# Kernel optimization log

Measured on AMD Instinct MI355X. Metric: run time of the kernel, lower is better.

Reference implementation:

```python
import jax, jax.numpy as jnp
import numpy as np

B, T, IN, H, O = 128, 512, 512, 512, 128

def setup_inputs() -> dict:
    key = jax.random.key(0)
    ks = jax.random.split(key, 16)
    s = 1.0 / np.sqrt(H)
    u = lambda k, shape: jax.random.uniform(k, shape, jnp.float32, -s, s)
    return {
        "x": jax.random.normal(ks[0], (B, T, IN), jnp.float32),
        # PyTorch GRU layer 0: weight_ih_l0 [3H, IN] (gate order r,z,n)
        "W_ih0": u(ks[1], (3 * H, IN)), "W_hh0": u(ks[2], (3 * H, H)),
        "b_ih0": u(ks[3], (3 * H,)),   "b_hh0": u(ks[4], (3 * H,)),
        # layer 1
        "W_ih1": u(ks[5], (3 * H, H)), "W_hh1": u(ks[6], (3 * H, H)),
        "b_ih1": u(ks[7], (3 * H,)),   "b_hh1": u(ks[8], (3 * H,)),
        # fc: Linear(H, O); fc_cate: Linear(O, 3O)
        "W_fc": u(ks[9], (O, H)),      "b_fc": u(ks[10], (O,)),
        "W_fcc": jax.random.uniform(ks[11], (3 * O, O), jnp.float32, -1/np.sqrt(O), 1/np.sqrt(O)),
        "b_fcc": jax.random.uniform(ks[12], (3 * O,), jnp.float32, -1/np.sqrt(O), 1/np.sqrt(O)),
    }

def _gru_layer(x, W_ih, W_hh, b_ih, b_hh):
    # x: [B, T, D] -> hidden sequence [B, T, H]. PyTorch gate order: r, z, n.
    Bm, Tm, _ = x.shape
    Hm = W_hh.shape[1]
    # precompute input projections for all timesteps: [B, T, 3H]
    xg = jnp.einsum('btd,gd->btg', x, W_ih) + b_ih
    b_hr, b_hz, b_hn = jnp.split(b_hh, 3)
    def step(h, xg_t):
        hg = h @ W_hh.T                       # [B, 3H]
        xr, xz, xn = jnp.split(xg_t, 3, axis=-1)
        hr, hz, hn = jnp.split(hg, 3, axis=-1)
        r = jax.nn.sigmoid(xr + hr + b_hr)
        z = jax.nn.sigmoid(xz + hz + b_hz)
        n = jnp.tanh(xn + r * (hn + b_hn))
        h_new = (1.0 - z) * n + z * h
        return h_new, h_new
    h0 = jnp.zeros((Bm, Hm), x.dtype)
    _, hs = jax.lax.scan(step, h0, jnp.swapaxes(xg, 0, 1))  # [T, B, H]
    return jnp.swapaxes(hs, 0, 1)

def reference(x, W_ih0, W_hh0, b_ih0, b_hh0, W_ih1, W_hh1, b_ih1, b_hh1, W_fc, b_fc, W_fcc, b_fcc):
    h1 = _gru_layer(x, W_ih0, W_hh0, b_ih0, b_hh0)   # layer 0 (dropout=0.0)
    h2 = _gru_layer(h1, W_ih1, W_hh1, b_ih1, b_hh1)  # layer 1
    out = h2[:, -1] @ W_fc.T + b_fc                  # [B, O]
    out_cate = out @ W_fcc.T + b_fcc                 # [B, 3O]
    return out[:, None, :], out_cate.reshape(-1, O, 3)
```

## Files before the change

kernel.cpp:

```cpp
#include <hip/hip_runtime.h>

#define Tn 512
#define Hn 512
#define HS 65536
#define NBLK 256

typedef __attribute__((ext_vector_type(8))) short s8v;
typedef __attribute__((ext_vector_type(4))) float f4v;
typedef __attribute__((ext_vector_type(4))) unsigned u4v;

__device__ __forceinline__ unsigned short f2bf(float f) {
  unsigned u = __float_as_uint(f);
  u = u + 0x7fffu + ((u >> 16) & 1u);
  return (unsigned short)(u >> 16);
}
__device__ __forceinline__ float bf2f(unsigned short s) {
  return __uint_as_float(((unsigned)s) << 16);
}
__device__ __forceinline__ float sigm(float v) { return 1.f / (1.f + __expf(-v)); }
__device__ __forceinline__ float tanh_f(float v) {
  v = fminf(fmaxf(v, -15.f), 15.f);
  float e = __expf(2.f * v);
  return (e - 1.f) / (e + 1.f);
}
__device__ __forceinline__ f4v mfma3(s8v ah, s8v al, s8v wh, s8v wl, f4v c) {
  c = __builtin_amdgcn_mfma_f32_16x16x32_bf16(ah, wh, c, 0, 0, 0);
  c = __builtin_amdgcn_mfma_f32_16x16x32_bf16(al, wh, c, 0, 0, 0);
  c = __builtin_amdgcn_mfma_f32_16x16x32_bf16(ah, wl, c, 0, 0, 0);
  return c;
}

__device__ __forceinline__ unsigned ld_mall(const unsigned* p) {
  return __hip_atomic_load(p, __ATOMIC_RELAXED, __HIP_MEMORY_SCOPE_AGENT);
}
__device__ __forceinline__ unsigned long long ld_mall64(const unsigned long long* p) {
  return __hip_atomic_load(p, __ATOMIC_RELAXED, __HIP_MEMORY_SCOPE_AGENT);
}
__device__ __forceinline__ void st_mall(unsigned* p, unsigned v) {
  __hip_atomic_store(p, v, __ATOMIC_RELAXED, __HIP_MEMORY_SCOPE_AGENT);
}

__device__ __forceinline__ void poll2(const int* pa, int ta, const int* pb2, int tb,
                                      int lane) {
  const int* p = (lane < 32) ? (pa + lane) : (pb2 + (lane - 32));
  const int tgt = (lane < 32) ? ta : tb;
  for (;;) {
    int v = (int)__hip_atomic_load(p, __ATOMIC_RELAXED, __HIP_MEMORY_SCOPE_AGENT);
    if (__all(v >= tgt)) break;
    __builtin_amdgcn_s_sleep(2);
  }
  asm volatile("" ::: "memory");
}

__global__ __launch_bounds__(256, 1) void gru_fused(
    const float* __restrict__ x,
    const float* __restrict__ Wih0, const float* __restrict__ Whh0,
    const float* __restrict__ bih0, const float* __restrict__ bhh0,
    const float* __restrict__ Wih1, const float* __restrict__ Whh1,
    const float* __restrict__ bih1, const float* __restrict__ bhh1,
    int* __restrict__ flags,
    unsigned* __restrict__ h1ring,
    unsigned* __restrict__ h2ring,
    float* __restrict__ h2fin) {
  __shared__ float part[2][3][64][25];

  const int tid = threadIdx.x, lane = tid & 63, wv = tid >> 6;
  const int kh = wv & 1, hs = wv >> 1;
  const int colr = lane & 15, kg = lane >> 4;

  const int bid = blockIdx.x;
  const int g = bid & 7;
  const int layer = g & 1;
  const int mq = g >> 1;
  const int jg = bid >> 3;
  const int col = jg * 16 + colr;

  const float* W = (layer == 0) ? (hs ? Whh0 : Wih0) : (hs ? Whh1 : Wih1);
  s8v wh[3][8], wl[3][8];
#pragma unroll
  for (int gg = 0; gg < 3; ++gg) {
    const float* wrow = W + (size_t)(gg * Hn + col) * Hn + kh * 256 + kg * 8;
#pragma unroll
    for (int ks = 0; ks < 8; ++ks) {
#pragma unroll
      for (int e = 0; e < 8; ++e) {
        float v = wrow[ks * 32 + e];
        unsigned short hi = f2bf(v);
        wh[gg][ks][e] = (short)hi;
        wl[gg][ks][e] = (short)f2bf(v - bf2f(hi));
      }
    }
  }

  float brz = 0, bzz = 0, bin = 0, bhn = 0;
  if (hs == 1 && kh == 0) {
    const float* bi = layer ? bih1 : bih0;
    const float* bb = layer ? bhh1 : bhh0;
    brz = bi[col] + bb[col];
    bzz = bi[Hn + col] + bb[Hn + col];
    bin = bi[2 * Hn + col];
    bhn = bb[2 * Hn + col];
  }

  const bool is_xw = (layer == 0 && hs == 0);

  float4 xp[2][8][2];
  if (is_xw) {
#pragma unroll
    for (int mt = 0; mt < 2; ++mt) {
      const int rowA = mq * 32 + mt * 16 + colr;
      const float* xq = x + ((size_t)rowA * Tn) * 512 + kh * 256 + kg * 8;
#pragma unroll
      for (int ks = 0; ks < 8; ++ks) {
        xp[mt][ks][0] = *(const float4*)(xq + ks * 32);
        xp[mt][ks][1] = *(const float4*)(xq + ks * 32 + 4);
      }
    }
  }

  int* const ownline = flags + g * 32;
  int* const l0line = flags + (mq * 2) * 32;
  int* const l1line = flags + (mq * 2 + 1) * 32;

  float hown[2][4] = {{0.f, 0.f, 0.f, 0.f}, {0.f, 0.f, 0.f, 0.f}};

#pragma unroll 1
  for (int t = 0; t < Tn; ++t) {
    const int pb = t & 1;

    if (hs == 1) {
      if (layer == 0) poll2(ownline, t, l1line, t - 3, lane);
      else            poll2(ownline, t, ownline, t, lane);
    } else if (layer == 1) {
      poll2(l0line, t + 1, l0line, t + 1, lane);
    }

    f4v acc[2][3];
#pragma unroll
    for (int mt = 0; mt < 2; ++mt)
#pragma unroll
      for (int gg = 0; gg < 3; ++gg) acc[mt][gg] = (f4v){0.f, 0.f, 0.f, 0.f};

    if (is_xw) {
#pragma unroll
      for (int mt = 0; mt < 2; ++mt) {
#pragma unroll
        for (int ks = 0; ks < 8; ++ks) {
          float v[8];
          v[0] = xp[mt][ks][0].x; v[1] = xp[mt][ks][0].y;
          v[2] = xp[mt][ks][0].z; v[3] = xp[mt][ks][0].w;
          v[4] = xp[mt][ks][1].x; v[5] = xp[mt][ks][1].y;
          v[6] = xp[mt][ks][1].z; v[7] = xp[mt][ks][1].w;
          u4v au, lu;
#pragma unroll
          for (int q = 0; q < 4; ++q) {
            unsigned u0 = __float_as_uint(v[2 * q]);
            unsigned u1 = __float_as_uint(v[2 * q + 1]);
            unsigned m0 = u0 & 0xffff0000u, m1 = u1 & 0xffff0000u;
            au[q] = (u0 >> 16) | m1;
            float l0 = v[2 * q] - __uint_as_float(m0);
            float l1 = v[2 * q + 1] - __uint_as_float(m1);
            lu[q] = (__float_as_uint(l0) >> 16) | (__float_as_uint(l1) & 0xffff0000u);
          }
          s8v ah = __builtin_bit_cast(s8v, au);
          s8v al = __builtin_bit_cast(s8v, lu);
#pragma unroll
          for (int gg = 0; gg < 3; ++gg)
            acc[mt][gg] = mfma3(ah, al, wh[gg][ks], wl[gg][ks], acc[mt][gg]);
        }
      }
      const int tpre = (t + 1 < Tn) ? (t + 1) : (Tn - 1);
#pragma unroll
      for (int mt = 0; mt < 2; ++mt) {
        const int rowA = mq * 32 + mt * 16 + colr;
        const float* xq = x + ((size_t)rowA * Tn + tpre) * 512 + kh * 256 + kg * 8;
#pragma unroll
        for (int ks = 0; ks < 8; ++ks) {
          xp[mt][ks][0] = *(const float4*)(xq + ks * 32);
          xp[mt][ks][1] = *(const float4*)(xq + ks * 32 + 4);
        }
      }
    } else {
      const unsigned* src;
      if (layer == 0)   src = h1ring + (size_t)((t - 1) & 3) * HS;
      else if (hs == 0) src = h1ring + (size_t)(t & 3) * HS;
      else              src = h2ring + (size_t)((t - 1) & 1) * HS;

#pragma unroll
      for (int mt = 0; mt < 2; ++mt) {
        const int rowA = mq * 32 + mt * 16 + colr;
        const unsigned long long* pb64 = (const unsigned long long*)
            (src + (size_t)rowA * 512 + kh * 256 + kg * 8);
        unsigned long long ub[32];
#pragma unroll
        for (int ks = 0; ks < 8; ++ks)
#pragma unroll
          for (int j = 0; j < 4; ++j)
            ub[ks * 4 + j] = ld_mall64(pb64 + ks * 16 + j);
#pragma unroll
        for (int ks = 0; ks < 8; ++ks) {
          u4v ahw, alw;
#pragma unroll
          for (int j = 0; j < 4; ++j) {
            unsigned a = (unsigned)ub[ks * 4 + j];
            unsigned b = (unsigned)(ub[ks * 4 + j] >> 32);
            ahw[j] = (a >> 16) | (b & 0xffff0000u);
            alw[j] = (a & 0xffffu) | (b << 16);
          }
          s8v AH = __builtin_bit_cast(s8v, ahw);
          s8v AL = __builtin_bit_cast(s8v, alw);
#pragma unroll
          for (int gg = 0; gg < 3; ++gg)
            acc[mt][gg] = mfma3(AH, AL, wh[gg][ks], wl[gg][ks], acc[mt][gg]);
        }
      }
    }

    const int widx = (hs == 0) ? kh : (kh == 1 ? 2 : -1);
    if (widx >= 0) {
#pragma unroll
      for (int mt = 0; mt < 2; ++mt)
#pragma unroll
        for (int gg = 0; gg < 3; ++gg)
#pragma unroll
          for (int r = 0; r < 4; ++r)
            part[pb][widx][lane][mt * 12 + gg * 4 + r] = acc[mt][gg][r];
    }
    __syncthreads();

    if (hs == 1 && kh == 0) {
      unsigned* od = layer ? (h2ring + (size_t)(t & 1) * HS)
                           : (h1ring + (size_t)(t & 3) * HS);
#pragma unroll
      for (int mt = 0; mt < 2; ++mt) {
#pragma unroll
        for (int r = 0; r < 4; ++r) {
          const int i0 = mt * 12 + r;
          float xr = part[pb][0][lane][i0]     + part[pb][1][lane][i0];
          float xz = part[pb][0][lane][i0 + 4] + part[pb][1][lane][i0 + 4];
          float xn = part[pb][0][lane][i0 + 8] + part[pb][1][lane][i0 + 8];
          float hr = acc[mt][0][r] + part[pb][2][lane][i0];
          float hz = acc[mt][1][r] + part[pb][2][lane][i0 + 4];
          float hn = acc[mt][2][r] + part[pb][2][lane][i0 + 8];
          float rr = sigm(xr + hr + brz);
          float zz = sigm(xz + hz + bzz);
          float nn = tanh_f(xn + bin + rr * (hn + bhn));
          float h = (1.f - zz) * nn + zz * hown[mt][r];
          hown[mt][r] = h;
          const int row = mq * 32 + mt * 16 + kg * 4 + r;
          unsigned short hi = f2bf(h);
          unsigned pk = ((unsigned)hi << 16) | (unsigned)f2bf(h - bf2f(hi));
          st_mall(od + (size_t)row * 512 + col, pk);
          if (layer == 1 && t == Tn - 1) h2fin[(size_t)row * 512 + col] = h;
        }
      }
      asm volatile("s_waitcnt vmcnt(0)" ::: "memory");
      if (lane == 0)
        st_mall((unsigned*)(ownline + jg), (unsigned)(t + 1));
    }
  }
}

__global__ __launch_bounds__(256) void fc_kernel(const float* __restrict__ h2,
                                                 const float* __restrict__ Wfc,
                                                 const float* __restrict__ bfc,
                                                 float* __restrict__ out) {
  int gid = blockIdx.x * 256 + threadIdx.x;
  int b = gid >> 7, o = gid & 127;
  const float* hp = h2 + (size_t)b * Hn;
  const float* wp = Wfc + (size_t)o * Hn;
  float acc = bfc[o];
#pragma unroll 8
  for (int k = 0; k < Hn; k += 4) {
    float4 h = *(const float4*)(hp + k);
    float4 w = *(const float4*)(wp + k);
    acc = fmaf(h.x, w.x, acc); acc = fmaf(h.y, w.y, acc);
    acc = fmaf(h.z, w.z, acc); acc = fmaf(h.w, w.w, acc);
  }
  out[gid] = acc;
}

__global__ __launch_bounds__(256) void fcc_kernel(const float* __restrict__ outv,
                                                  const float* __restrict__ Wfcc,
                                                  const float* __restrict__ bfcc,
                                                  float* __restrict__ oc) {
  int gid = blockIdx.x * 256 + threadIdx.x;
  int b = gid / 384, g = gid - b * 384;
  const float* op = outv + (size_t)b * 128;
  const float* wp = Wfcc + (size_t)g * 128;
  float acc = bfcc[g];
#pragma unroll 8
  for (int k = 0; k < 128; k += 4) {
    float4 o4 = *(const float4*)(op + k);
    float4 w4 = *(const float4*)(wp + k);
    acc = fmaf(o4.x, w4.x, acc); acc = fmaf(o4.y, w4.y, acc);
    acc = fmaf(o4.z, w4.z, acc); acc = fmaf(o4.w, w4.w, acc);
  }
  oc[gid] = acc;
}

extern "C" void kernel_launch(void* const* d_in, const int* in_sizes, int n_in,
                              void* d_out, int out_size, void* d_ws, size_t ws_size,
                              hipStream_t stream) {
  (void)in_sizes; (void)n_in; (void)out_size; (void)ws_size;
  const float* x    = (const float*)d_in[0];
  const float* Wih0 = (const float*)d_in[1];
  const float* Whh0 = (const float*)d_in[2];
  const float* bih0 = (const float*)d_in[3];
  const float* bhh0 = (const float*)d_in[4];
  const float* Wih1 = (const float*)d_in[5];
  const float* Whh1 = (const float*)d_in[6];
  const float* bih1 = (const float*)d_in[7];
  const float* bhh1 = (const float*)d_in[8];
  const float* Wfc  = (const float*)d_in[9];
  const float* bfc  = (const float*)d_in[10];
  const float* Wfcc = (const float*)d_in[11];
  const float* bfcc = (const float*)d_in[12];

  char* w = (char*)d_ws;
  int* flags = (int*)w;
  unsigned* h1ring = (unsigned*)(w + 8192);
  unsigned* h2ring = h1ring + 4 * HS;
  float* h2fin = (float*)(h2ring + 2 * HS);
  const size_t total = 8192 + (size_t)4 * HS * 4 + (size_t)2 * HS * 4 + (size_t)HS * 4;

  hipMemsetAsync(d_ws, 0, total, stream);

  gru_fused<<<NBLK, 256, 0, stream>>>(x, Wih0, Whh0, bih0, bhh0,
                                      Wih1, Whh1, bih1, bhh1,
                                      flags, h1ring, h2ring, h2fin);

  float* out = (float*)d_out;
  fc_kernel<<<64, 256, 0, stream>>>(h2fin, Wfc, bfc, out);
  fcc_kernel<<<192, 256, 0, stream>>>(out, Wfcc, bfcc, out + 16384);
}
```

Before: 5.982 ms.

## Split GRU recurrent GEMV K-dimension across eight waves per block

Doubles the block from 4 to 8 wavefronts. The input and hidden projections are each split into four K-chunks of 128 instead of two of 256, so every wave does half the MFMA and load work on the serial per-timestep critical path. A single combiner wave now sums seven partials from shared memory before the gate math. The poll sleep is also shortened. The trade-off is higher register pressure per thread, since launch bounds are now 512, plus more LDS traffic and reduction work in the combiner.

```diff
diff --git a/kernel.cpp b/kernel.cpp
--- a/kernel.cpp
+++ b/kernel.cpp
@@ -30,9 +30,6 @@
   return c;
 }
 
-__device__ __forceinline__ unsigned ld_mall(const unsigned* p) {
-  return __hip_atomic_load(p, __ATOMIC_RELAXED, __HIP_MEMORY_SCOPE_AGENT);
-}
 __device__ __forceinline__ unsigned long long ld_mall64(const unsigned long long* p) {
   return __hip_atomic_load(p, __ATOMIC_RELAXED, __HIP_MEMORY_SCOPE_AGENT);
 }
@@ -47,12 +44,12 @@
   for (;;) {
     int v = (int)__hip_atomic_load(p, __ATOMIC_RELAXED, __HIP_MEMORY_SCOPE_AGENT);
     if (__all(v >= tgt)) break;
-    __builtin_amdgcn_s_sleep(2);
+    __builtin_amdgcn_s_sleep(1);
   }
   asm volatile("" ::: "memory");
 }
 
-__global__ __launch_bounds__(256, 1) void gru_fused(
+__global__ __launch_bounds__(512, 1) void gru_fused(
     const float* __restrict__ x,
     const float* __restrict__ Wih0, const float* __restrict__ Whh0,
     const float* __restrict__ bih0, const float* __restrict__ bhh0,
@@ -62,10 +59,12 @@
     unsigned* __restrict__ h1ring,
     unsigned* __restrict__ h2ring,
     float* __restrict__ h2fin) {
-  __shared__ float part[2][3][64][25];
+  __shared__ float part[2][7][64][25];
 
   const int tid = threadIdx.x, lane = tid & 63, wv = tid >> 6;
-  const int kh = wv & 1, hs = wv >> 1;
+  const bool inside = (wv < 4);
+  const int kq = wv & 3;
+  const bool comb = (wv == 4);
   const int colr = lane & 15, kg = lane >> 4;
 
   const int bid = blockIdx.x;
@@ -75,13 +74,13 @@
   const int jg = bid >> 3;
   const int col = jg * 16 + colr;
 
-  const float* W = (layer == 0) ? (hs ? Whh0 : Wih0) : (hs ? Whh1 : Wih1);
-  s8v wh[3][8], wl[3][8];
+  const float* W = (layer == 0) ? (inside ? Wih0 : Whh0) : (inside ? Wih1 : Whh1);
+  s8v wh[3][4], wl[3][4];
 #pragma unroll
   for (int gg = 0; gg < 3; ++gg) {
-    const float* wrow = W + (size_t)(gg * Hn + col) * Hn + kh * 256 + kg * 8;
-#pragma unroll
-    for (int ks = 0; ks < 8; ++ks) {
+    const float* wrow = W + (size_t)(gg * Hn + col) * Hn + kq * 128 + kg * 8;
+#pragma unroll
+    for (int ks = 0; ks < 4; ++ks) {
 #pragma unroll
       for (int e = 0; e < 8; ++e) {
         float v = wrow[ks * 32 + e];
@@ -93,7 +92,7 @@
   }
 
   float brz = 0, bzz = 0, bin = 0, bhn = 0;
-  if (hs == 1 && kh == 0) {
+  if (comb) {
     const float* bi = layer ? bih1 : bih0;
     const float* bb = layer ? bhh1 : bhh0;
     brz = bi[col] + bb[col];
@@ -102,16 +101,16 @@
     bhn = bb[2 * Hn + col];
   }
 
-  const bool is_xw = (layer == 0 && hs == 0);
-
-  float4 xp[2][8][2];
+  const bool is_xw = (layer == 0 && inside);
+
+  float4 xp[2][4][2];
   if (is_xw) {
 #pragma unroll
     for (int mt = 0; mt < 2; ++mt) {
       const int rowA = mq * 32 + mt * 16 + colr;
-      const float* xq = x + ((size_t)rowA * Tn) * 512 + kh * 256 + kg * 8;
-#pragma unroll
-      for (int ks = 0; ks < 8; ++ks) {
+      const float* xq = x + ((size_t)rowA * Tn) * 512 + kq * 128 + kg * 8;
+#pragma unroll
+      for (int ks = 0; ks < 4; ++ks) {
         xp[mt][ks][0] = *(const float4*)(xq + ks * 32);
         xp[mt][ks][1] = *(const float4*)(xq + ks * 32 + 4);
       }
@@ -128,11 +127,14 @@
   for (int t = 0; t < Tn; ++t) {
     const int pb = t & 1;
 
-    if (hs == 1) {
-      if (layer == 0) poll2(ownline, t, l1line, t - 3, lane);
-      else            poll2(ownline, t, ownline, t, lane);
-    } else if (layer == 1) {
-      poll2(l0line, t + 1, l0line, t + 1, lane);
+    if (layer == 0) {
+      if (!inside) {
+        if (comb) poll2(ownline, t, l1line, t - 3, lane);
+        else      poll2(ownline, t, ownline, t, lane);
+      }
+    } else {
+      if (inside) poll2(l0line, t + 1, l0line, t + 1, lane);
+      else        poll2(ownline, t, ownline, t, lane);
     }
 
     f4v acc[2][3];
@@ -145,7 +147,7 @@
 #pragma unroll
       for (int mt = 0; mt < 2; ++mt) {
 #pragma unroll
-        for (int ks = 0; ks < 8; ++ks) {
+        for (int ks = 0; ks < 4; ++ks) {
           float v[8];
           v[0] = xp[mt][ks][0].x; v[1] = xp[mt][ks][0].y;
           v[2] = xp[mt][ks][0].z; v[3] = xp[mt][ks][0].w;
@@ -173,37 +175,37 @@
 #pragma unroll
       for (int mt = 0; mt < 2; ++mt) {
         const int rowA = mq * 32 + mt * 16 + colr;
-        const float* xq = x + ((size_t)rowA * Tn + tpre) * 512 + kh * 256 + kg * 8;
-#pragma unroll
-        for (int ks = 0; ks < 8; ++ks) {
+        const float* xq = x + ((size_t)rowA * Tn + tpre) * 512 + kq * 128 + kg * 8;
+#pragma unroll
+        for (int ks = 0; ks < 4; ++ks) {
           xp[mt][ks][0] = *(const float4*)(xq + ks * 32);
           xp[mt][ks][1] = *(const float4*)(xq + ks * 32 + 4);
         }
       }
     } else {
       const unsigned* src;
-      if (layer == 0)   src = h1ring + (size_t)((t - 1) & 3) * HS;
-      else if (hs == 0) src = h1ring + (size_t)(t & 3) * HS;
-      else              src = h2ring + (size_t)((t - 1) & 1) * HS;
-
+      if (layer == 0)  src = h1ring + (size_t)((t - 1) & 3) * HS;
+      else if (inside) src = h1ring + (size_t)(t & 3) * HS;
+      else             src = h2ring + (size_t)((t - 1) & 1) * HS;
+
+      unsigned long long ub[2][16];
 #pragma unroll
       for (int mt = 0; mt < 2; ++mt) {
         const int rowA = mq * 32 + mt * 16 + colr;
         const unsigned long long* pb64 = (const unsigned long long*)
-            (src + (size_t)rowA * 512 + kh * 256 + kg * 8);
-        unsigned long long ub[32];
-#pragma unroll
-        for (int ks = 0; ks < 8; ++ks)
-#pragma unroll
-          for (int j = 0; j < 4; ++j)
-            ub[ks * 4 + j] = ld_mall64(pb64 + ks * 16 + j);
-#pragma unroll
-        for (int ks = 0; ks < 8; ++ks) {
+            (src + (size_t)rowA * 512 + kq * 128 + kg * 8);
+#pragma unroll
+        for (int i = 0; i < 16; ++i) ub[mt][i] = ld_mall64(pb64 + (i >> 2) * 16 + (i & 3));
+      }
+#pragma unroll
+      for (int mt = 0; mt < 2; ++mt) {
+#pragma unroll
+        for (int ks = 0; ks < 4; ++ks) {
           u4v ahw, alw;
 #pragma unroll
           for (int j = 0; j < 4; ++j) {
-            unsigned a = (unsigned)ub[ks * 4 + j];
-            unsigned b = (unsigned)(ub[ks * 4 + j] >> 32);
+            unsigned a = (unsigned)ub[mt][ks * 4 + j];
+            unsigned b = (unsigned)(ub[mt][ks * 4 + j] >> 32);
             ahw[j] = (a >> 16) | (b & 0xffff0000u);
             alw[j] = (a & 0xffffu) | (b << 16);
           }
@@ -216,19 +218,19 @@
       }
     }
 
-    const int widx = (hs == 0) ? kh : (kh == 1 ? 2 : -1);
-    if (widx >= 0) {
+    if (!comb) {
+      const int slot = inside ? kq : (3 + kq);
 #pragma unroll
       for (int mt = 0; mt < 2; ++mt)
 #pragma unroll
         for (int gg = 0; gg < 3; ++gg)
 #pragma unroll
           for (int r = 0; r < 4; ++r)
-            part[pb][widx][lane][mt * 12 + gg * 4 + r] = acc[mt][gg][r];
+            part[pb][slot][lane][mt * 12 + gg * 4 + r] = acc[mt][gg][r];
     }
     __syncthreads();
 
-    if (hs == 1 && kh == 0) {
+    if (comb) {
       unsigned* od = layer ? (h2ring + (size_t)(t & 1) * HS)
                            : (h1ring + (size_t)(t & 3) * HS);
 #pragma unroll
@@ -236,12 +238,18 @@
 #pragma unroll
         for (int r = 0; r < 4; ++r) {
           const int i0 = mt * 12 + r;
-          float xr = part[pb][0][lane][i0]     + part[pb][1][lane][i0];
-          float xz = part[pb][0][lane][i0 + 4] + part[pb][1][lane][i0 + 4];
-          float xn = part[pb][0][lane][i0 + 8] + part[pb][1][lane][i0 + 8];
-          float hr = acc[mt][0][r] + part[pb][2][lane][i0];
-          float hz = acc[mt][1][r] + part[pb][2][lane][i0 + 4];
-          float hn = acc[mt][2][r] + part[pb][2][lane][i0 + 8];
+          float xr = part[pb][0][lane][i0] + part[pb][1][lane][i0]
+                   + part[pb][2][lane][i0] + part[pb][3][lane][i0];
+          float xz = part[pb][0][lane][i0 + 4] + part[pb][1][lane][i0 + 4]
+                   + part[pb][2][lane][i0 + 4] + part[pb][3][lane][i0 + 4];
+          float xn = part[pb][0][lane][i0 + 8] + part[pb][1][lane][i0 + 8]
+                   + part[pb][2][lane][i0 + 8] + part[pb][3][lane][i0 + 8];
+          float hr = acc[mt][0][r] + part[pb][4][lane][i0]
+                   + part[pb][5][lane][i0] + part[pb][6][lane][i0];
+          float hz = acc[mt][1][r] + part[pb][4][lane][i0 + 4]
+                   + part[pb][5][lane][i0 + 4] + part[pb][6][lane][i0 + 4];
+          float hn = acc[mt][2][r] + part[pb][4][lane][i0 + 8]
+                   + part[pb][5][lane][i0 + 8] + part[pb][6][lane][i0 + 8];
           float rr = sigm(xr + hr + brz);
           float zz = sigm(xz + hz + bzz);
           float nn = tanh_f(xn + bin + rr * (hn + bhn));
@@ -326,7 +334,7 @@
 
   hipMemsetAsync(d_ws, 0, total, stream);
 
-  gru_fused<<<NBLK, 256, 0, stream>>>(x, Wih0, Whh0, bih0, bhh0,
+  gru_fused<<<NBLK, 512, 0, stream>>>(x, Wih0, Whh0, bih0, bhh0,
                                       Wih1, Whh1, bih1, bhh1,
                                       flags, h1ring, h2ring, h2fin);
 
```

New measurement: 7.550 ms. 26.2% more time.

## Split GRU recurrence K-dim across 16 waves and use atomic counter sync

Applied to the files above, without the earlier changes.

Each block grows from 4 to 16 waves, and the K dimension of each matmul is split 8 ways per side. This cuts the per-wave serial MFMA chain and per-wave register pressure for the weights. Two combiner waves each handle one m-tile and reduce 15 partials from LDS. The 32-lane per-block flag polling is replaced by one atomic fetch_add counter per group, polled by a single wave and followed by a block barrier. The aim is lower per-step latency on the serial recurrence, paid for with more LDS reduction, an extra __syncthreads per step, and contention on the atomic counter.

```diff
diff --git a/kernel.cpp b/kernel.cpp
--- a/kernel.cpp
+++ b/kernel.cpp
@@ -8,6 +8,7 @@
 typedef __attribute__((ext_vector_type(8))) short s8v;
 typedef __attribute__((ext_vector_type(4))) float f4v;
 typedef __attribute__((ext_vector_type(4))) unsigned u4v;
+typedef unsigned long long ull;
 
 __device__ __forceinline__ unsigned short f2bf(float f) {
   unsigned u = __float_as_uint(f);
@@ -30,42 +31,30 @@
   return c;
 }
 
-__device__ __forceinline__ unsigned ld_mall(const unsigned* p) {
-  return __hip_atomic_load(p, __ATOMIC_RELAXED, __HIP_MEMORY_SCOPE_AGENT);
-}
-__device__ __forceinline__ unsigned long long ld_mall64(const unsigned long long* p) {
+__device__ __forceinline__ ull ld_mall64(const ull* p) {
   return __hip_atomic_load(p, __ATOMIC_RELAXED, __HIP_MEMORY_SCOPE_AGENT);
 }
 __device__ __forceinline__ void st_mall(unsigned* p, unsigned v) {
   __hip_atomic_store(p, v, __ATOMIC_RELAXED, __HIP_MEMORY_SCOPE_AGENT);
 }
 
-__device__ __forceinline__ void poll2(const int* pa, int ta, const int* pb2, int tb,
-                                      int lane) {
-  const int* p = (lane < 32) ? (pa + lane) : (pb2 + (lane - 32));
-  const int tgt = (lane < 32) ? ta : tb;
-  for (;;) {
-    int v = (int)__hip_atomic_load(p, __ATOMIC_RELAXED, __HIP_MEMORY_SCOPE_AGENT);
-    if (__all(v >= tgt)) break;
-    __builtin_amdgcn_s_sleep(2);
-  }
-  asm volatile("" ::: "memory");
-}
-
-__global__ __launch_bounds__(256, 1) void gru_fused(
+__global__ __launch_bounds__(1024, 1) void gru_fused(
     const float* __restrict__ x,
     const float* __restrict__ Wih0, const float* __restrict__ Whh0,
     const float* __restrict__ bih0, const float* __restrict__ bhh0,
     const float* __restrict__ Wih1, const float* __restrict__ Whh1,
     const float* __restrict__ bih1, const float* __restrict__ bhh1,
-    int* __restrict__ flags,
+    int* __restrict__ cnt,
     unsigned* __restrict__ h1ring,
     unsigned* __restrict__ h2ring,
     float* __restrict__ h2fin) {
-  __shared__ float part[2][3][64][25];
+  __shared__ float part[16][64][28];
 
   const int tid = threadIdx.x, lane = tid & 63, wv = tid >> 6;
-  const int kh = wv & 1, hs = wv >> 1;
+  const bool hside = (wv < 8);
+  const int kq = wv & 7;
+  const bool comb0 = (wv == 8), comb1 = (wv == 12);
+  const bool iscomb = comb0 || comb1;
   const int colr = lane & 15, kg = lane >> 4;
 
   const int bid = blockIdx.x;
@@ -75,13 +64,13 @@
   const int jg = bid >> 3;
   const int col = jg * 16 + colr;
 
-  const float* W = (layer == 0) ? (hs ? Whh0 : Wih0) : (hs ? Whh1 : Wih1);
-  s8v wh[3][8], wl[3][8];
+  const float* W = hside ? (layer ? Whh1 : Whh0) : (layer ? Wih1 : Wih0);
+  s8v wh[3][2], wl[3][2];
 #pragma unroll
   for (int gg = 0; gg < 3; ++gg) {
-    const float* wrow = W + (size_t)(gg * Hn + col) * Hn + kh * 256 + kg * 8;
-#pragma unroll
-    for (int ks = 0; ks < 8; ++ks) {
+    const float* wrow = W + (size_t)(gg * Hn + col) * Hn + kq * 64 + kg * 8;
+#pragma unroll
+    for (int ks = 0; ks < 2; ++ks) {
 #pragma unroll
       for (int e = 0; e < 8; ++e) {
         float v = wrow[ks * 32 + e];
@@ -93,7 +82,7 @@
   }
 
   float brz = 0, bzz = 0, bin = 0, bhn = 0;
-  if (hs == 1 && kh == 0) {
+  if (iscomb) {
     const float* bi = layer ? bih1 : bih0;
     const float* bb = layer ? bhh1 : bhh0;
     brz = bi[col] + bb[col];
@@ -102,38 +91,42 @@
     bhn = bb[2 * Hn + col];
   }
 
-  const bool is_xw = (layer == 0 && hs == 0);
-
-  float4 xp[2][8][2];
+  const bool is_xw = (layer == 0 && !hside);
+
+  float4 xp[2][2][2];
   if (is_xw) {
 #pragma unroll
     for (int mt = 0; mt < 2; ++mt) {
       const int rowA = mq * 32 + mt * 16 + colr;
-      const float* xq = x + ((size_t)rowA * Tn) * 512 + kh * 256 + kg * 8;
-#pragma unroll
-      for (int ks = 0; ks < 8; ++ks) {
+      const float* xq = x + ((size_t)rowA * Tn) * 512 + kq * 64 + kg * 8;
+#pragma unroll
+      for (int ks = 0; ks < 2; ++ks) {
         xp[mt][ks][0] = *(const float4*)(xq + ks * 32);
         xp[mt][ks][1] = *(const float4*)(xq + ks * 32 + 4);
       }
     }
   }
 
-  int* const ownline = flags + g * 32;
-  int* const l0line = flags + (mq * 2) * 32;
-  int* const l1line = flags + (mq * 2 + 1) * 32;
-
-  float hown[2][4] = {{0.f, 0.f, 0.f, 0.f}, {0.f, 0.f, 0.f, 0.f}};
+  int* const owncnt = cnt + g * 32;
+  int* const peercnt = cnt + (g ^ 1) * 32;
+
+  float hown[4] = {0.f, 0.f, 0.f, 0.f};
 
 #pragma unroll 1
   for (int t = 0; t < Tn; ++t) {
-    const int pb = t & 1;
-
-    if (hs == 1) {
-      if (layer == 0) poll2(ownline, t, l1line, t - 3, lane);
-      else            poll2(ownline, t, ownline, t, lane);
-    } else if (layer == 1) {
-      poll2(l0line, t + 1, l0line, t + 1, lane);
-    }
+    if (wv == 0) {
+      const int ta = 64 * t;
+      const int tb = layer ? 64 * (t + 1) : 64 * (t - 3);
+      const int* p = (lane < 32) ? owncnt : peercnt;
+      const int tgt = (lane < 32) ? ta : tb;
+      for (;;) {
+        int v = __hip_atomic_load(p, __ATOMIC_RELAXED, __HIP_MEMORY_SCOPE_AGENT);
+        if (__all(v >= tgt)) break;
+        __builtin_amdgcn_s_sleep(4);
+      }
+      asm volatile("" ::: "memory");
+    }
+    __syncthreads();
 
     f4v acc[2][3];
 #pragma unroll
@@ -145,7 +138,7 @@
 #pragma unroll
       for (int mt = 0; mt < 2; ++mt) {
 #pragma unroll
-        for (int ks = 0; ks < 8; ++ks) {
+        for (int ks = 0; ks < 2; ++ks) {
           float v[8];
           v[0] = xp[mt][ks][0].x; v[1] = xp[mt][ks][0].y;
           v[2] = xp[mt][ks][0].z; v[3] = xp[mt][ks][0].w;
@@ -173,37 +166,36 @@
 #pragma unroll
       for (int mt = 0; mt < 2; ++mt) {
         const int rowA = mq * 32 + mt * 16 + colr;
-        const float* xq = x + ((size_t)rowA * Tn + tpre) * 512 + kh * 256 + kg * 8;
-#pragma unroll
-        for (int ks = 0; ks < 8; ++ks) {
+        const float* xq = x + ((size_t)rowA * Tn + tpre) * 512 + kq * 64 + kg * 8;
+#pragma unroll
+        for (int ks = 0; ks < 2; ++ks) {
           xp[mt][ks][0] = *(const float4*)(xq + ks * 32);
           xp[mt][ks][1] = *(const float4*)(xq + ks * 32 + 4);
         }
       }
     } else {
       const unsigned* src;
-      if (layer == 0)   src = h1ring + (size_t)((t - 1) & 3) * HS;
-      else if (hs == 0) src = h1ring + (size_t)(t & 3) * HS;
-      else              src = h2ring + (size_t)((t - 1) & 1) * HS;
-
+      if (!hside)     src = h1ring + (size_t)(t & 3) * HS;
+      else if (layer) src = h2ring + (size_t)((t - 1) & 1) * HS;
+      else            src = h1ring + (size_t)((t - 1) & 3) * HS;
+
+      ull ub[2][8];
 #pragma unroll
       for (int mt = 0; mt < 2; ++mt) {
         const int rowA = mq * 32 + mt * 16 + colr;
-        const unsigned long long* pb64 = (const unsigned long long*)
-            (src + (size_t)rowA * 512 + kh * 256 + kg * 8);
-        unsigned long long ub[32];
-#pragma unroll
-        for (int ks = 0; ks < 8; ++ks)
-#pragma unroll
-          for (int j = 0; j < 4; ++j)
-            ub[ks * 4 + j] = ld_mall64(pb64 + ks * 16 + j);
-#pragma unroll
-        for (int ks = 0; ks < 8; ++ks) {
+        const ull* pb64 = (const ull*)(src + (size_t)rowA * 512 + kq * 64 + kg * 8);
+#pragma unroll
+        for (int i = 0; i < 8; ++i) ub[mt][i] = ld_mall64(pb64 + (i >> 2) * 16 + (i & 3));
+      }
+#pragma unroll
+      for (int mt = 0; mt < 2; ++mt) {
+#pragma unroll
+        for (int ks = 0; ks < 2; ++ks) {
           u4v ahw, alw;
 #pragma unroll
           for (int j = 0; j < 4; ++j) {
-            unsigned a = (unsigned)ub[ks * 4 + j];
-            unsigned b = (unsigned)(ub[ks * 4 + j] >> 32);
+            unsigned a = (unsigned)ub[mt][ks * 4 + j];
+            unsigned b = (unsigned)(ub[mt][ks * 4 + j] >> 32);
             ahw[j] = (a >> 16) | (b & 0xffff0000u);
             alw[j] = (a & 0xffffu) | (b << 16);
           }
@@ -216,47 +208,56 @@
       }
     }
 
-    const int widx = (hs == 0) ? kh : (kh == 1 ? 2 : -1);
-    if (widx >= 0) {
+    if (!iscomb) {
 #pragma unroll
       for (int mt = 0; mt < 2; ++mt)
 #pragma unroll
         for (int gg = 0; gg < 3; ++gg)
-#pragma unroll
-          for (int r = 0; r < 4; ++r)
-            part[pb][widx][lane][mt * 12 + gg * 4 + r] = acc[mt][gg][r];
+          *(f4v*)&part[wv][lane][mt * 12 + gg * 4] = acc[mt][gg];
+    } else {
+      const int omt = comb0 ? 1 : 0;
+#pragma unroll
+      for (int gg = 0; gg < 3; ++gg)
+        *(f4v*)&part[wv][lane][omt * 12 + gg * 4] = acc[omt][gg];
     }
     __syncthreads();
 
-    if (hs == 1 && kh == 0) {
+    if (iscomb) {
+      const int mt = comb0 ? 0 : 1;
+      const int off = mt * 12;
+      f4v xs[3], hs[3];
+#pragma unroll
+      for (int gg = 0; gg < 3; ++gg) { xs[gg] = acc[mt][gg]; hs[gg] = (f4v){0,0,0,0}; }
+#pragma unroll
+      for (int s = 0; s < 8; ++s)
+#pragma unroll
+        for (int gg = 0; gg < 3; ++gg)
+          hs[gg] += *(const f4v*)&part[s][lane][off + gg * 4];
+#pragma unroll
+      for (int s = 8; s < 16; ++s) {
+        if (s == (comb0 ? 8 : 12)) continue;
+#pragma unroll
+        for (int gg = 0; gg < 3; ++gg)
+          xs[gg] += *(const f4v*)&part[s][lane][off + gg * 4];
+      }
       unsigned* od = layer ? (h2ring + (size_t)(t & 1) * HS)
                            : (h1ring + (size_t)(t & 3) * HS);
 #pragma unroll
-      for (int mt = 0; mt < 2; ++mt) {
-#pragma unroll
-        for (int r = 0; r < 4; ++r) {
-          const int i0 = mt * 12 + r;
-          float xr = part[pb][0][lane][i0]     + part[pb][1][lane][i0];
-          float xz = part[pb][0][lane][i0 + 4] + part[pb][1][lane][i0 + 4];
-          float xn = part[pb][0][lane][i0 + 8] + part[pb][1][lane][i0 + 8];
-          float hr = acc[mt][0][r] + part[pb][2][lane][i0];
-          float hz = acc[mt][1][r] + part[pb][2][lane][i0 + 4];
-          float hn = acc[mt][2][r] + part[pb][2][lane][i0 + 8];
-          float rr = sigm(xr + hr + brz);
-          float zz = sigm(xz + hz + bzz);
-          float nn = tanh_f(xn + bin + rr * (hn + bhn));
-          float h = (1.f - zz) * nn + zz * hown[mt][r];
-          hown[mt][r] = h;
-          const int row = mq * 32 + mt * 16 + kg * 4 + r;
-          unsigned short hi = f2bf(h);
-          unsigned pk = ((unsigned)hi << 16) | (unsigned)f2bf(h - bf2f(hi));
-          st_mall(od + (size_t)row * 512 + col, pk);
-          if (layer == 1 && t == Tn - 1) h2fin[(size_t)row * 512 + col] = h;
-        }
+      for (int r = 0; r < 4; ++r) {
+        float rr = sigm(xs[0][r] + hs[0][r] + brz);
+        float zz = sigm(xs[1][r] + hs[1][r] + bzz);
+        float nn = tanh_f(xs[2][r] + bin + rr * (hs[2][r] + bhn));
+        float h = (1.f - zz) * nn + zz * hown[r];
+        hown[r] = h;
+        const int row = mq * 32 + mt * 16 + kg * 4 + r;
+        unsigned short hi = f2bf(h);
+        unsigned pk = ((unsigned)hi << 16) | (unsigned)f2bf(h - bf2f(hi));
+        st_mall(od + (size_t)row * 512 + col, pk);
+        if (layer == 1 && t == Tn - 1) h2fin[(size_t)row * 512 + col] = h;
       }
       asm volatile("s_waitcnt vmcnt(0)" ::: "memory");
       if (lane == 0)
-        st_mall((unsigned*)(ownline + jg), (unsigned)(t + 1));
+        __hip_atomic_fetch_add(owncnt, 1, __ATOMIC_RELAXED, __HIP_MEMORY_SCOPE_AGENT);
     }
   }
 }
@@ -318,7 +319,7 @@
   const float* bfcc = (const float*)d_in[12];
 
   char* w = (char*)d_ws;
-  int* flags = (int*)w;
+  int* cnt = (int*)w;
   unsigned* h1ring = (unsigned*)(w + 8192);
   unsigned* h2ring = h1ring + 4 * HS;
   float* h2fin = (float*)(h2ring + 2 * HS);
@@ -326,9 +327,9 @@
 
   hipMemsetAsync(d_ws, 0, total, stream);
 
-  gru_fused<<<NBLK, 256, 0, stream>>>(x, Wih0, Whh0, bih0, bhh0,
-                                      Wih1, Whh1, bih1, bhh1,
-                                      flags, h1ring, h2ring, h2fin);
+  gru_fused<<<NBLK, 1024, 0, stream>>>(x, Wih0, Whh0, bih0, bhh0,
+                                       Wih1, Whh1, bih1, bhh1,
+                                       cnt, h1ring, h2ring, h2fin);
 
   float* out = (float*)d_out;
   fc_kernel<<<64, 256, 0, stream>>>(h2fin, Wfc, bfc, out);
```

Result: slower. 11.29 ms (+88.7%).
